# Kernel tuning notes

Hardware: AMD Instinct MI355X
Metric: run time of the kernel (lower is better)

Reference implementation:

```python
import jax, jax.numpy as jnp
import numpy as np

H, HKV, DH, T_MAX = 32, 8, 128, 4096
ROPE_BASE = 500000.0


def apply_rope(x, pos, base):
    # x: [B, h, T, D]; MLX rope, traditional=False (split-half rotation)
    B, h, T, D = x.shape
    half = D // 2
    inv_freq = 1.0 / (base ** (jnp.arange(half, dtype=jnp.float32) * 2.0 / D))
    t = (pos + jnp.arange(T)).astype(jnp.float32)  # absolute positions
    ang = t[:, None] * inv_freq[None, :]           # [T, half]
    cos = jnp.cos(ang)[None, None]                 # [1,1,T,half]
    sin = jnp.sin(ang)[None, None]
    x1, x2 = x[..., :half], x[..., half:]
    return jnp.concatenate([x1 * cos - x2 * sin, x2 * cos + x1 * sin], axis=-1)


def setup_inputs() -> dict:
    key = jax.random.key(0)
    ks = jax.random.split(key, 5)
    hidden = 4096
    return {
        "hidden_states": jax.random.normal(ks[0], (1, 2048, hidden), jnp.float32),
        "Wq": jax.random.normal(ks[1], (hidden, H * DH), jnp.float32) * 0.02,
        "Wk": jax.random.normal(ks[2], (hidden, HKV * DH), jnp.float32) * 0.02,
        "Wv": jax.random.normal(ks[3], (hidden, HKV * DH), jnp.float32) * 0.02,
        "Wo": jax.random.normal(ks[4], (H * DH, hidden), jnp.float32) * 0.02,
        "pos_int": 0,
    }


def reference(hidden_states, Wq, Wk, Wv, Wo, pos_int):
    B, T, _ = hidden_states.shape
    q = (hidden_states @ Wq).reshape(B, T, H, DH).transpose(0, 2, 1, 3)    # [B,H,T,D]
    k = (hidden_states @ Wk).reshape(B, T, HKV, DH).transpose(0, 2, 1, 3)  # [B,Hkv,T,D]
    v = (hidden_states @ Wv).reshape(B, T, HKV, DH).transpose(0, 2, 1, 3)

    q = apply_rope(q, pos_int, ROPE_BASE)
    k = apply_rope(k, pos_int, ROPE_BASE)

    # KV cache: write at [pos:pos+T], then slice [:pos+T] (pos is static Python int)
    k_cache = jnp.zeros((B, HKV, T_MAX, DH), jnp.float32)
    v_cache = jnp.zeros((B, HKV, T_MAX, DH), jnp.float32)
    k_cache = jax.lax.dynamic_update_slice(k_cache, k, (0, 0, pos_int, 0))
    v_cache = jax.lax.dynamic_update_slice(v_cache, v, (0, 0, pos_int, 0))
    end_pos = pos_int + T
    k_ = k_cache[:, :, :end_pos, :]  # [B,Hkv,S,D]
    v_ = v_cache[:, :, :end_pos, :]
    S = end_pos

    # GQA without materializing repeat_interleave: group query heads per kv head
    group = H // HKV
    qg = q.reshape(B, HKV, group, T, DH)
    scale = 1.0 / jnp.sqrt(jnp.float32(DH))
    scores = jnp.einsum("bhgtd,bhsd->bhgts", qg, k_) * scale  # [B,Hkv,g,T,S]
    # torch SDPA is_causal=True: top-left aligned mask (allow s <= t)
    causal = jnp.arange(S)[None, :] <= jnp.arange(T)[:, None]  # [T,S]
    scores = jnp.where(causal[None, None, None], scores, -jnp.inf)
    probs = jax.nn.softmax(scores, axis=-1)
    attn = jnp.einsum("bhgts,bhsd->bhgtd", probs, v_)          # [B,Hkv,g,T,D]
    attn = attn.reshape(B, H, T, DH).transpose(0, 2, 1, 3).reshape(B, T, H * DH)
    return attn @ Wo
```

## Files before the change

kernel.cpp:

```cpp
#include <hip/hip_runtime.h>
#include <hip/hip_bf16.h>
#include <math.h>

typedef unsigned short u16;
typedef __attribute__((ext_vector_type(4))) float f32x4;
typedef __attribute__((ext_vector_type(8))) short bf16x8;

#define GLD16(gptr, lptr) __builtin_amdgcn_global_load_lds( \
    (const __attribute__((address_space(1))) void*)(gptr),  \
    (__attribute__((address_space(3))) void*)(lptr), 16, 0, 0)

__device__ __forceinline__ float bf2f(u16 u) {
  union { unsigned int i; float f; } c; c.i = ((unsigned int)u) << 16; return c.f;
}
__device__ __forceinline__ u16 f2bf(float f) {
  union { float f; unsigned int i; } c; c.f = f;
  unsigned int r = c.i + 0x7fffu + ((c.i >> 16) & 1u);
  return (u16)(r >> 16);
}

__global__ __launch_bounds__(256) void f32_to_bf16(const float* __restrict__ in,
                                                   u16* __restrict__ out, int n4) {
  int i = blockIdx.x * 256 + threadIdx.x;
  if (i >= n4) return;
  float4 v = reinterpret_cast<const float4*>(in)[i];
  ushort4 o;
  o.x = f2bf(v.x); o.y = f2bf(v.y); o.z = f2bf(v.z); o.w = f2bf(v.w);
  reinterpret_cast<ushort4*>(out)[i] = o;
}

__global__ __launch_bounds__(256) void transpose_convert(const float* __restrict__ W,
                                                         u16* __restrict__ Wt,
                                                         int K, int N) {
  __shared__ float tile[32][33];
  const int n0 = blockIdx.x * 32, k0 = blockIdx.y * 32;
  const int tx = threadIdx.x & 31, ty = threadIdx.x >> 5;
#pragma unroll
  for (int r = 0; r < 32; r += 8)
    tile[ty + r][tx] = W[(size_t)(k0 + ty + r) * N + (n0 + tx)];
  __syncthreads();
#pragma unroll
  for (int r = 0; r < 32; r += 8)
    Wt[(size_t)(n0 + ty + r) * K + (k0 + tx)] = f2bf(tile[tx][ty + r]);
}

__global__ __launch_bounds__(256) void transpose_v(const u16* __restrict__ Vsrc,
                                                   u16* __restrict__ Vt) {
  __shared__ u16 tile[32][33];
  const int t0 = blockIdx.x * 32, d0 = blockIdx.y * 32, hkv = blockIdx.z;
  const int tx = threadIdx.x & 31, ty = threadIdx.x >> 5;
#pragma unroll
  for (int r = 0; r < 32; r += 8)
    tile[ty + r][tx] = Vsrc[(size_t)(t0 + ty + r) * 6144 + hkv * 128 + d0 + tx];
  __syncthreads();
#pragma unroll
  for (int r = 0; r < 32; r += 8)
    Vt[((size_t)hkv * 128 + d0 + ty + r) * 2048 + t0 + tx] = tile[tx][ty + r];
}

__global__ __launch_bounds__(256) void rope_table(float2* __restrict__ tab,
                                                  const int* __restrict__ pos_ptr) {
  int idx = blockIdx.x * 256 + threadIdx.x;
  int d = idx & 63, t = idx >> 6;
  int pos = *pos_ptr;
  float inv = exp2f(-(float)d * (0.015625f * 18.931568569324174f));
  float ang = (float)(pos + t) * inv;
  tab[idx] = make_float2(cosf(ang), sinf(ang));
}

__global__ __launch_bounds__(256) void rope_apply(u16* __restrict__ X, int nheads,
                                                  int stride,
                                                  const float2* __restrict__ tab) {
  int idx = blockIdx.x * 256 + threadIdx.x;
  int total = 2048 * nheads * 64;
  if (idx >= total) return;
  int d = idx & 63;
  int h = (idx >> 6) % nheads;
  int t = idx / (64 * nheads);
  float2 cs = tab[t * 64 + d];
  size_t base = (size_t)t * stride + h * 128 + d;
  float x1 = bf2f(X[base]);
  float x2 = bf2f(X[base + 64]);
  X[base]      = f2bf(x1 * cs.x - x2 * cs.y);
  X[base + 64] = f2bf(x2 * cs.x + x1 * cs.y);
}

template <int BN, int OUT_BF16>
__global__ __launch_bounds__(512, 2) void gemm_big(const u16* __restrict__ A,
                                                   const u16* __restrict__ Bt,
                                                   void* __restrict__ C,
                                                   int M, int N, int K,
                                                   int ntiles, size_t zstride) {
  constexpr int NF = BN / 64;
  constexpr int WCOL = BN / 4;
  constexpr int LB = BN / 64;
  __shared__ alignas(16) u16 As[2][256 * 64];
  __shared__ alignas(16) u16 Bs[2][BN * 64];
  const int tid = threadIdx.x;
  const int lane = tid & 63, wid = tid >> 6;
  const int l15 = lane & 15, lg = lane >> 4;
  const int wm = wid >> 2, wn = wid & 3;
  const int wvb = tid & ~63;
  const int z = blockIdx.z;
  const int ko = z * ntiles * 64;

  const int id0 = blockIdx.y * gridDim.x + blockIdx.x;
  const int xcd = id0 & 7;
  const int l = id0 >> 3;
  const int m0 = (l & 7) * 256;
  const int n0 = (xcd * (gridDim.x >> 3) + (l >> 3)) * BN;

  f32x4 acc[8][NF];
#pragma unroll
  for (int i = 0; i < 8; ++i)
#pragma unroll
    for (int j = 0; j < NF; ++j) {
      f32x4 zz = {0.f, 0.f, 0.f, 0.f};
      acc[i][j] = zz;
    }

#define STAGE(s_, b_)                                                           \
  do {                                                                          \
    _Pragma("unroll")                                                           \
    for (int p = 0; p < 4; ++p) {                                               \
      const int slot = p * 512 + tid;                                           \
      const int row = slot >> 3, ch = slot & 7;                                 \
      const int col = (ch ^ (row & 7)) * 8;                                     \
      GLD16(A + (size_t)(m0 + row) * K + ko + (s_) * 64 + col,                  \
            &As[b_][(p * 512 + wvb) * 8]);                                      \
    }                                                                           \
    _Pragma("unroll")                                                           \
    for (int p = 0; p < LB; ++p) {                                              \
      const int slot = p * 512 + tid;                                           \
      const int row = slot >> 3, ch = slot & 7;                                 \
      const int col = (ch ^ (row & 7)) * 8;                                     \
      GLD16(Bt + (size_t)(n0 + row) * K + ko + (s_) * 64 + col,                 \
            &Bs[b_][(p * 512 + wvb) * 8]);                                      \
    }                                                                           \
  } while (0)

  STAGE(0, 0);
  __syncthreads();
  int cur = 0;

  for (int t = 0; t < ntiles; ++t) {
    if (t + 1 < ntiles) STAGE(t + 1, cur ^ 1);
#pragma unroll
    for (int g = 0; g < 2; ++g) {
      bf16x8 af[8], bfr[NF];
#pragma unroll
      for (int i = 0; i < 8; ++i) {
        const int row = wm * 128 + i * 16 + l15;
        const int ch = (g * 4 + lg) ^ (row & 7);
        af[i] = *reinterpret_cast<const bf16x8*>(&As[cur][row * 64 + ch * 8]);
      }
#pragma unroll
      for (int j = 0; j < NF; ++j) {
        const int row = wn * WCOL + j * 16 + l15;
        const int ch = (g * 4 + lg) ^ (row & 7);
        bfr[j] = *reinterpret_cast<const bf16x8*>(&Bs[cur][row * 64 + ch * 8]);
      }
      __builtin_amdgcn_s_setprio(1);
#pragma unroll
      for (int i = 0; i < 8; ++i)
#pragma unroll
        for (int j = 0; j < NF; ++j)
          acc[i][j] = __builtin_amdgcn_mfma_f32_16x16x32_bf16(af[i], bfr[j], acc[i][j], 0, 0, 0);
      __builtin_amdgcn_s_setprio(0);
    }
    __syncthreads();
    cur ^= 1;
  }
#undef STAGE

  u16* Cb = (u16*)C + (size_t)z * zstride;
#pragma unroll
  for (int i = 0; i < 8; ++i)
#pragma unroll
    for (int j = 0; j < NF; ++j)
#pragma unroll
      for (int r = 0; r < 4; ++r) {
        const int row = m0 + wm * 128 + i * 16 + lg * 4 + r;
        const int col = n0 + wn * WCOL + j * 16 + l15;
        const float v = acc[i][j][r];
        if (OUT_BF16) Cb[(size_t)row * N + col] = f2bf(v);
        else          ((float*)C)[(size_t)row * N + col] = v;
      }
}

__global__ __launch_bounds__(256) void wo_reduce(const u16* __restrict__ P,
                                                 float* __restrict__ out) {
  const size_t i = ((size_t)blockIdx.x * 256 + threadIdx.x) * 8;
  bf16x8 a = *reinterpret_cast<const bf16x8*>(P + i);
  bf16x8 b = *reinterpret_cast<const bf16x8*>(P + 8388608 + i);
  float4 o0, o1;
  o0.x = bf2f((u16)a[0]) + bf2f((u16)b[0]);
  o0.y = bf2f((u16)a[1]) + bf2f((u16)b[1]);
  o0.z = bf2f((u16)a[2]) + bf2f((u16)b[2]);
  o0.w = bf2f((u16)a[3]) + bf2f((u16)b[3]);
  o1.x = bf2f((u16)a[4]) + bf2f((u16)b[4]);
  o1.y = bf2f((u16)a[5]) + bf2f((u16)b[5]);
  o1.z = bf2f((u16)a[6]) + bf2f((u16)b[6]);
  o1.w = bf2f((u16)a[7]) + bf2f((u16)b[7]);
  *reinterpret_cast<float4*>(out + i) = o0;
  *reinterpret_cast<float4*>(out + i + 4) = o1;
}

__global__ __launch_bounds__(512) void attn_kernel(const u16* __restrict__ Q,
                                                   const u16* __restrict__ K,
                                                   const u16* __restrict__ Vt,
                                                   u16* __restrict__ O,
                                                   const int* __restrict__ pos_ptr) {
  const int pos = *pos_ptr;
  const int h = blockIdx.y;
  const int hkv = h >> 2;
  const int tid = threadIdx.x;
  const int w = tid >> 6, lane = tid & 63;
  const int l15 = lane & 15, lg = lane >> 4;

  __shared__ alignas(16) u16 Ks[2][64 * 128];
  __shared__ alignas(16) u16 Vs[2][128 * 64];
  __shared__ alignas(16) u16 Pl[8][16][72];

  const u16* Kh = K + hkv * 128;
  const u16* Vh = Vt + (size_t)hkv * 128 * 2048;

  const float C = 0.12752961957823275f;
  const float THR = 62.0f;
  const int wvb = tid & ~63;

#define STAGE_TILE(st_, b_)                                                        \
  do {                                                                             \
    const int s0_ = (st_) * 64;                                                    \
    _Pragma("unroll")                                                              \
    for (int p = 0; p < 2; ++p) {                                                  \
      const int idx = p * 512 + tid;                                               \
      const int kr = idx >> 4, kc = (idx & 15) ^ (kr & 7);                         \
      GLD16(Kh + (size_t)(s0_ + kr) * 6144 + kc * 8, &Ks[b_][(p * 512 + wvb) * 8]);\
      const int vr = idx >> 3, vc = (idx & 7) ^ (vr & 7);                          \
      GLD16(Vh + (size_t)vr * 2048 + s0_ + vc * 8, &Vs[b_][(p * 512 + wvb) * 8]);  \
    }                                                                              \
  } while (0)

  for (int pass = 0; pass < 2; ++pass) {
    const int qb = (pass == 0) ? (8 + (int)blockIdx.x) : (7 - (int)blockIdx.x);
    const int qt0 = qb * 128;
    const int nst = 2 * qb + 2;
    const int frag_base = qt0 + w * 16;

    bf16x8 qa[4];
#pragma unroll
    for (int kk = 0; kk < 4; ++kk)
      qa[kk] = *reinterpret_cast<const bf16x8*>(
          Q + (size_t)(frag_base + l15) * 6144 + h * 128 + kk * 32 + lg * 8);

    f32x4 acc[8];
#pragma unroll
    for (int i = 0; i < 8; ++i) { f32x4 z = {0.f, 0.f, 0.f, 0.f}; acc[i] = z; }
    float mrun[4], lpart[4];
#pragma unroll
    for (int r = 0; r < 4; ++r) {
      mrun[r] = (pos > 0) ? 0.0f : -INFINITY;
      lpart[r] = 0.0f;
    }

    STAGE_TILE(0, 0);
    __syncthreads();
    int cur = 0;

    for (int st = 0; st < nst; ++st) {
      if (st + 1 < nst) STAGE_TILE(st + 1, cur ^ 1);
      const int s0 = st * 64;

      float pv[4][4];
      __builtin_amdgcn_s_setprio(1);
#pragma unroll
      for (int sub = 0; sub < 4; ++sub) {
        f32x4 s4 = {0.f, 0.f, 0.f, 0.f};
        const int row = sub * 16 + l15;
#pragma unroll
        for (int kk = 0; kk < 4; ++kk) {
          const int chunk = (kk * 4 + lg) ^ (row & 7);
          bf16x8 kf = *reinterpret_cast<const bf16x8*>(&Ks[cur][row * 128 + chunk * 8]);
          s4 = __builtin_amdgcn_mfma_f32_16x16x32_bf16(qa[kk], kf, s4, 0, 0, 0);
        }
#pragma unroll
        for (int r = 0; r < 4; ++r) pv[sub][r] = s4[r];
      }
      __builtin_amdgcn_s_setprio(0);

      if (s0 + 64 > frag_base) {
#pragma unroll
        for (int r = 0; r < 4; ++r) {
          const int qrow = frag_base + lg * 4 + r;
#pragma unroll
          for (int sub = 0; sub < 4; ++sub) {
            const int scol = s0 + sub * 16 + l15;
            pv[sub][r] = (scol <= qrow) ? pv[sub][r] : -INFINITY;
          }
        }
      }

      float lmax[4];
#pragma unroll
      for (int r = 0; r < 4; ++r)
        lmax[r] = fmaxf(fmaxf(pv[0][r], pv[1][r]), fmaxf(pv[2][r], pv[3][r]));
      float dml = fmaxf(fmaxf(lmax[0] - mrun[0], lmax[1] - mrun[1]),
                        fmaxf(lmax[2] - mrun[2], lmax[3] - mrun[3]));
      if (!__all(dml <= THR)) {
        float sfr[4];
#pragma unroll
        for (int r = 0; r < 4; ++r) {
          float mx = lmax[r];
#pragma unroll
          for (int off = 1; off < 16; off <<= 1) mx = fmaxf(mx, __shfl_xor(mx, off));
          const float mnew = fmaxf(mrun[r], mx);
          sfr[r] = exp2f((mrun[r] - mnew) * C);
          mrun[r] = mnew;
          lpart[r] *= sfr[r];
        }
#pragma unroll
        for (int dc = 0; dc < 8; ++dc)
#pragma unroll
          for (int r = 0; r < 4; ++r) acc[dc][r] *= sfr[r];
      }

#pragma unroll
      for (int r = 0; r < 4; ++r) {
        const float nmC = -mrun[r] * C;
        float ps = 0.0f;
#pragma unroll
        for (int sub = 0; sub < 4; ++sub) {
          const float p = exp2f(fmaf(pv[sub][r], C, nmC));
          pv[sub][r] = p;
          ps += p;
        }
        lpart[r] += ps;
      }

#pragma unroll
      for (int sub = 0; sub < 4; ++sub)
#pragma unroll
        for (int r = 0; r < 4; ++r)
          Pl[w][lg * 4 + r][sub * 16 + l15] = f2bf(pv[sub][r]);

      __builtin_amdgcn_s_setprio(1);
#pragma unroll
      for (int ks = 0; ks < 2; ++ks) {
        bf16x8 pf = *reinterpret_cast<const bf16x8*>(&Pl[w][l15][ks * 32 + lg * 8]);
#pragma unroll
        for (int dc = 0; dc < 8; ++dc) {
          const int row = dc * 16 + l15;
          const int chunk = (ks * 4 + lg) ^ (row & 7);
          bf16x8 vf = *reinterpret_cast<const bf16x8*>(&Vs[cur][row * 64 + chunk * 8]);
          acc[dc] = __builtin_amdgcn_mfma_f32_16x16x32_bf16(pf, vf, acc[dc], 0, 0, 0);
        }
      }
      __builtin_amdgcn_s_setprio(0);

      __syncthreads();
      cur ^= 1;
    }

#pragma unroll
    for (int r = 0; r < 4; ++r) {
      float l = lpart[r];
#pragma unroll
      for (int off = 1; off < 16; off <<= 1) l += __shfl_xor(l, off);
      if (pos > 0) l += (float)pos * exp2f(-mrun[r] * C);
      const float linv = 1.0f / l;
      const int qrow = frag_base + lg * 4 + r;
#pragma unroll
      for (int dc = 0; dc < 8; ++dc)
        O[(size_t)qrow * 4096 + h * 128 + dc * 16 + l15] = f2bf(acc[dc][r] * linv);
    }
  }
#undef STAGE_TILE
}

extern "C" void kernel_launch(void* const* d_in, const int* in_sizes, int n_in,
                              void* d_out, int out_size, void* d_ws, size_t ws_size,
                              hipStream_t stream) {
  const float* hs = (const float*)d_in[0];
  const float* Wq = (const float*)d_in[1];
  const float* Wk = (const float*)d_in[2];
  const float* Wv = (const float*)d_in[3];
  const float* Wo = (const float*)d_in[4];
  const int* pos  = (const int*)d_in[5];

  char* ws = (char*)d_ws;
  u16* hs_bf = (u16*)(ws + 0);
  u16* WT    = (u16*)(ws + 16777216ULL);
  u16* QKVb  = (u16*)(ws + 67108864ULL);
  u16* attnO = hs_bf;
  u16* WoT   = WT;
  u16* Vtg   = (u16*)(ws + 50331648ULL);
  float2* tabF = (float2*)(ws + 54525952ULL);
  u16* Ppart = (u16*)(ws + 50331648ULL);

  f32_to_bf16<<<8192, 256, 0, stream>>>(hs, hs_bf, 2097152);
  transpose_convert<<<dim3(128, 128), 256, 0, stream>>>(Wq, WT, 4096, 4096);
  transpose_convert<<<dim3(32, 128), 256, 0, stream>>>(Wk, WT + (size_t)4096 * 4096, 4096, 1024);
  transpose_convert<<<dim3(32, 128), 256, 0, stream>>>(Wv, WT + (size_t)5120 * 4096, 4096, 1024);

  gemm_big<192, 1><<<dim3(32, 8, 1), 512, 0, stream>>>(hs_bf, WT, QKVb, 2048, 6144, 4096, 64, 0);

  transpose_convert<<<dim3(128, 128), 256, 0, stream>>>(Wo, WoT, 4096, 4096);

  rope_table<<<512, 256, 0, stream>>>(tabF, pos);
  rope_apply<<<16384, 256, 0, stream>>>(QKVb, 32, 6144, tabF);
  rope_apply<<<4096, 256, 0, stream>>>(QKVb + 4096, 8, 6144, tabF);

  transpose_v<<<dim3(64, 4, 8), 256, 0, stream>>>(QKVb + 5120, Vtg);

  attn_kernel<<<dim3(8, 32), 512, 0, stream>>>(QKVb, QKVb + 4096, Vtg, attnO, pos);

  gemm_big<256, 1><<<dim3(16, 8, 2), 512, 0, stream>>>(attnO, WoT, Ppart, 2048, 4096, 4096,
                                                       32, 8388608);
  wo_reduce<<<4096, 256, 0, stream>>>(Ppart, (float*)d_out);
}
```

Measured before the change: 341.0 us.

## Shrink GEMM M-tile to 128 and drop split-K for output projection

```diff
diff --git a/kernel.cpp b/kernel.cpp
--- a/kernel.cpp
+++ b/kernel.cpp
@@ -86,33 +86,31 @@
 }
 
 template <int BN, int OUT_BF16>
-__global__ __launch_bounds__(512, 2) void gemm_big(const u16* __restrict__ A,
+__global__ __launch_bounds__(512, 4) void gemm_2cu(const u16* __restrict__ A,
                                                    const u16* __restrict__ Bt,
                                                    void* __restrict__ C,
-                                                   int M, int N, int K,
-                                                   int ntiles, size_t zstride) {
+                                                   int M, int N, int K) {
   constexpr int NF = BN / 64;
   constexpr int WCOL = BN / 4;
   constexpr int LB = BN / 64;
-  __shared__ alignas(16) u16 As[2][256 * 64];
+  __shared__ alignas(16) u16 As[2][128 * 64];
   __shared__ alignas(16) u16 Bs[2][BN * 64];
   const int tid = threadIdx.x;
   const int lane = tid & 63, wid = tid >> 6;
   const int l15 = lane & 15, lg = lane >> 4;
   const int wm = wid >> 2, wn = wid & 3;
   const int wvb = tid & ~63;
-  const int z = blockIdx.z;
-  const int ko = z * ntiles * 64;
-
+
+  const int gy = gridDim.y;
   const int id0 = blockIdx.y * gridDim.x + blockIdx.x;
   const int xcd = id0 & 7;
   const int l = id0 >> 3;
-  const int m0 = (l & 7) * 256;
-  const int n0 = (xcd * (gridDim.x >> 3) + (l >> 3)) * BN;
-
-  f32x4 acc[8][NF];
-#pragma unroll
-  for (int i = 0; i < 8; ++i)
+  const int m0 = (l % gy) * 128;
+  const int n0 = (xcd * (gridDim.x >> 3) + l / gy) * BN;
+
+  f32x4 acc[4][NF];
+#pragma unroll
+  for (int i = 0; i < 4; ++i)
 #pragma unroll
     for (int j = 0; j < NF; ++j) {
       f32x4 zz = {0.f, 0.f, 0.f, 0.f};
@@ -122,11 +120,11 @@
 #define STAGE(s_, b_)                                                           \
   do {                                                                          \
     _Pragma("unroll")                                                           \
-    for (int p = 0; p < 4; ++p) {                                               \
+    for (int p = 0; p < 2; ++p) {                                               \
       const int slot = p * 512 + tid;                                           \
       const int row = slot >> 3, ch = slot & 7;                                 \
       const int col = (ch ^ (row & 7)) * 8;                                     \
-      GLD16(A + (size_t)(m0 + row) * K + ko + (s_) * 64 + col,                  \
+      GLD16(A + (size_t)(m0 + row) * K + (s_) * 64 + col,                       \
             &As[b_][(p * 512 + wvb) * 8]);                                      \
     }                                                                           \
     _Pragma("unroll")                                                           \
@@ -134,7 +132,7 @@
       const int slot = p * 512 + tid;                                           \
       const int row = slot >> 3, ch = slot & 7;                                 \
       const int col = (ch ^ (row & 7)) * 8;                                     \
-      GLD16(Bt + (size_t)(n0 + row) * K + ko + (s_) * 64 + col,                 \
+      GLD16(Bt + (size_t)(n0 + row) * K + (s_) * 64 + col,                      \
             &Bs[b_][(p * 512 + wvb) * 8]);                                      \
     }                                                                           \
   } while (0)
@@ -143,14 +141,15 @@
   __syncthreads();
   int cur = 0;
 
-  for (int t = 0; t < ntiles; ++t) {
-    if (t + 1 < ntiles) STAGE(t + 1, cur ^ 1);
+  const int nt = K >> 6;
+  for (int t = 0; t < nt; ++t) {
+    if (t + 1 < nt) STAGE(t + 1, cur ^ 1);
 #pragma unroll
     for (int g = 0; g < 2; ++g) {
-      bf16x8 af[8], bfr[NF];
-#pragma unroll
-      for (int i = 0; i < 8; ++i) {
-        const int row = wm * 128 + i * 16 + l15;
+      bf16x8 af[4], bfr[NF];
+#pragma unroll
+      for (int i = 0; i < 4; ++i) {
+        const int row = wm * 64 + i * 16 + l15;
         const int ch = (g * 4 + lg) ^ (row & 7);
         af[i] = *reinterpret_cast<const bf16x8*>(&As[cur][row * 64 + ch * 8]);
       }
@@ -162,7 +161,7 @@
       }
       __builtin_amdgcn_s_setprio(1);
 #pragma unroll
-      for (int i = 0; i < 8; ++i)
+      for (int i = 0; i < 4; ++i)
 #pragma unroll
         for (int j = 0; j < NF; ++j)
           acc[i][j] = __builtin_amdgcn_mfma_f32_16x16x32_bf16(af[i], bfr[j], acc[i][j], 0, 0, 0);
@@ -173,37 +172,18 @@
   }
 #undef STAGE
 
-  u16* Cb = (u16*)C + (size_t)z * zstride;
-#pragma unroll
-  for (int i = 0; i < 8; ++i)
+#pragma unroll
+  for (int i = 0; i < 4; ++i)
 #pragma unroll
     for (int j = 0; j < NF; ++j)
 #pragma unroll
       for (int r = 0; r < 4; ++r) {
-        const int row = m0 + wm * 128 + i * 16 + lg * 4 + r;
+        const int row = m0 + wm * 64 + i * 16 + lg * 4 + r;
         const int col = n0 + wn * WCOL + j * 16 + l15;
         const float v = acc[i][j][r];
-        if (OUT_BF16) Cb[(size_t)row * N + col] = f2bf(v);
+        if (OUT_BF16) ((u16*)C)[(size_t)row * N + col] = f2bf(v);
         else          ((float*)C)[(size_t)row * N + col] = v;
       }
-}
-
-__global__ __launch_bounds__(256) void wo_reduce(const u16* __restrict__ P,
-                                                 float* __restrict__ out) {
-  const size_t i = ((size_t)blockIdx.x * 256 + threadIdx.x) * 8;
-  bf16x8 a = *reinterpret_cast<const bf16x8*>(P + i);
-  bf16x8 b = *reinterpret_cast<const bf16x8*>(P + 8388608 + i);
-  float4 o0, o1;
-  o0.x = bf2f((u16)a[0]) + bf2f((u16)b[0]);
-  o0.y = bf2f((u16)a[1]) + bf2f((u16)b[1]);
-  o0.z = bf2f((u16)a[2]) + bf2f((u16)b[2]);
-  o0.w = bf2f((u16)a[3]) + bf2f((u16)b[3]);
-  o1.x = bf2f((u16)a[4]) + bf2f((u16)b[4]);
-  o1.y = bf2f((u16)a[5]) + bf2f((u16)b[5]);
-  o1.z = bf2f((u16)a[6]) + bf2f((u16)b[6]);
-  o1.w = bf2f((u16)a[7]) + bf2f((u16)b[7]);
-  *reinterpret_cast<float4*>(out + i) = o0;
-  *reinterpret_cast<float4*>(out + i + 4) = o1;
 }
 
 __global__ __launch_bounds__(512) void attn_kernel(const u16* __restrict__ Q,
@@ -396,14 +376,13 @@
   u16* WoT   = WT;
   u16* Vtg   = (u16*)(ws + 50331648ULL);
   float2* tabF = (float2*)(ws + 54525952ULL);
-  u16* Ppart = (u16*)(ws + 50331648ULL);
 
   f32_to_bf16<<<8192, 256, 0, stream>>>(hs, hs_bf, 2097152);
   transpose_convert<<<dim3(128, 128), 256, 0, stream>>>(Wq, WT, 4096, 4096);
   transpose_convert<<<dim3(32, 128), 256, 0, stream>>>(Wk, WT + (size_t)4096 * 4096, 4096, 1024);
   transpose_convert<<<dim3(32, 128), 256, 0, stream>>>(Wv, WT + (size_t)5120 * 4096, 4096, 1024);
 
-  gemm_big<192, 1><<<dim3(32, 8, 1), 512, 0, stream>>>(hs_bf, WT, QKVb, 2048, 6144, 4096, 64, 0);
+  gemm_2cu<192, 1><<<dim3(32, 16), 512, 0, stream>>>(hs_bf, WT, QKVb, 2048, 6144, 4096);
 
   transpose_convert<<<dim3(128, 128), 256, 0, stream>>>(Wo, WoT, 4096, 4096);
 
@@ -415,7 +394,5 @@
 
   attn_kernel<<<dim3(8, 32), 512, 0, stream>>>(QKVb, QKVb + 4096, Vtg, attnO, pos);
 
-  gemm_big<256, 1><<<dim3(16, 8, 2), 512, 0, stream>>>(attnO, WoT, Ppart, 2048, 4096, 4096,
-                                                       32, 8388608);
-  wo_reduce<<<4096, 256, 0, stream>>>(Ppart, (float*)d_out);
-}
+  gemm_2cu<128, 0><<<dim3(32, 16), 512, 0, stream>>>(attnO, WoT, d_out, 2048, 4096, 4096);
+}
```

Result: no change. 342.5 us (+0.4%).
